# Optimization experiments

Measured on AMD Instinct MI355X. Metric: run time of the kernel, lower is better.

Reference implementation:

```python
import jax, jax.numpy as jnp
import numpy as np

NUM_HEADS = 16


def setup_inputs() -> dict:
    key = jax.random.key(0)
    ks = jax.random.split(key, 7)
    B, L, H = 4, 1370, 1024
    s = 0.02
    return {
        "hidden_states": jax.random.normal(ks[0], (B, L, H), jnp.float32),
        "Wq": jax.random.normal(ks[1], (H, H), jnp.float32) * s,
        "bq": jax.random.normal(ks[2], (H,), jnp.float32) * s,
        "Wk": jax.random.normal(ks[3], (H, H), jnp.float32) * s,
        "bk": jax.random.normal(ks[4], (H,), jnp.float32) * s,
        "Wv": jax.random.normal(ks[5], (H, H), jnp.float32) * s,
        "bv": jax.random.normal(ks[6], (H,), jnp.float32) * s,
    }


def reference(hidden_states, Wq, bq, Wk, bk, Wv, bv):
    B, L, hidden = hidden_states.shape
    n_heads = NUM_HEADS
    d = hidden // n_heads  # head_dim = 64

    def split_heads(x):  # [B,L,hidden] -> [B,H,L,d]
        return x.reshape(B, L, n_heads, d).transpose(0, 2, 1, 3)

    # torch Linear: y = x @ W^T + b
    q = split_heads(hidden_states @ Wq.T + bq)
    k = split_heads(hidden_states @ Wk.T + bk)
    v = split_heads(hidden_states @ Wv.T + bv)

    scale = 1.0 / jnp.sqrt(jnp.asarray(d, hidden_states.dtype))
    # attn_bias is all-zeros (no causal mask, no head_mask) -> omitted
    scores = jnp.einsum("bhld,bhsd->bhls", q, k) * scale  # [B,H,L,S]
    attn = jax.nn.softmax(scores, axis=-1)
    # dropout_p = 0.0 (eval mode), callback is None
    ctx = jnp.einsum("bhls,bhsd->bhld", attn, v)  # [B,H,L,d]
    ctx = ctx.transpose(0, 2, 1, 3).reshape(B, L, hidden)
    return ctx
```

## Files before the change

### kernel.cpp

```cpp
#include <hip/hip_runtime.h>

#define B_    4
#define L_    1370
#define NH_   16
#define D_    64
#define HID_  1024
#define M_    (B_ * L_)
#define LPAD  1408

#define XB_OFF  0u
#define WB_OFF  5611520u
#define QW_OFF  8757248u
#define KW_OFF  14524416u
#define VT_OFF  20291584u

typedef __attribute__((ext_vector_type(8))) short bf16x8;
typedef __attribute__((ext_vector_type(4))) short bf16x4;
typedef __attribute__((ext_vector_type(4))) float f32x4;
typedef __attribute__((ext_vector_type(2))) unsigned int u32x2;

#define LOG2E   1.44269504089f
#define QSCALE  0.18033688011f
#define SOFT_M2 14.4269504089f

__device__ __forceinline__ unsigned short f2bf(float f) {
  unsigned int u = __builtin_bit_cast(unsigned int, f);
  u += 0x7FFFu + ((u >> 16) & 1u);
  return (unsigned short)(u >> 16);
}

__device__ __forceinline__ float fexp2(float x) {
#if __has_builtin(__builtin_amdgcn_exp2f)
  return __builtin_amdgcn_exp2f(x);
#else
  return exp2f(x);
#endif
}

__device__ __forceinline__ unsigned int pkbf(float a, float b) {
#if __has_builtin(__builtin_amdgcn_cvt_pk_bf16_f32)
  auto r = __builtin_amdgcn_cvt_pk_bf16_f32(a, b);
  return __builtin_bit_cast(unsigned int, r);
#else
  return (unsigned int)f2bf(a) | ((unsigned int)f2bf(b) << 16);
#endif
}

#define GLOAD16(gp, lp)                                                    \
  __builtin_amdgcn_global_load_lds(                                        \
      (const __attribute__((address_space(1))) unsigned int*)(gp),         \
      (__attribute__((address_space(3))) unsigned int*)(lp), 16, 0, 0)

#define XN4 ((M_ * HID_) / 4)
#define WN4 ((HID_ * HID_) / 4)
#define TOT4 (XN4 + 3 * WN4)

__global__ void cvt_all(const float* __restrict__ hs,
                        const float* __restrict__ Wq,
                        const float* __restrict__ Wk,
                        const float* __restrict__ Wv,
                        unsigned short* __restrict__ ws) {
  int i4 = blockIdx.x * 256 + threadIdx.x;
  if (i4 >= TOT4) return;
  const float* src;
  unsigned short* dst;
  if (i4 < XN4) {
    src = hs + (size_t)i4 * 4;
    dst = ws + XB_OFF + (size_t)i4 * 4;
  } else {
    int j = i4 - XN4;
    int w = j >> 18;
    int jj = j & (WN4 - 1);
    src = (w == 0 ? Wq : w == 1 ? Wk : Wv) + (size_t)jj * 4;
    dst = ws + WB_OFF + (size_t)w * (HID_ * HID_) + (size_t)jj * 4;
  }
  float4 v = *(const float4*)src;
  bf16x4 o;
  o[0] = (short)f2bf(v.x); o[1] = (short)f2bf(v.y);
  o[2] = (short)f2bf(v.z); o[3] = (short)f2bf(v.w);
  *(bf16x4*)dst = o;
}

__global__ __launch_bounds__(256)
void qkv_gemm(const unsigned short* __restrict__ XB,
              const unsigned short* __restrict__ WB,
              const float* __restrict__ bq,
              const float* __restrict__ bk,
              const float* __restrict__ bv,
              unsigned short* __restrict__ ws) {
  __shared__ unsigned short smem[16384];
  unsigned short* lA = smem;
  unsigned short* lB = smem + 8192;

  const int x = blockIdx.x;
  const int b = (x >= 33) ? 3 : (x >= 22) ? 2 : (x >= 11) ? 1 : 0;
  const int j = x - 11 * b;
  const int z = blockIdx.z;
  const int n0 = blockIdx.y * 128;

  const unsigned short* W = WB + (size_t)z * (HID_ * HID_);
  const float* bias = (z == 0) ? bq : (z == 1) ? bk : bv;
  const float scale = (z == 0) ? QSCALE : 1.0f;

  const int tid = threadIdx.x;
  const int lane = tid & 63;
  const int wv = tid >> 6;
  const int l15 = lane & 15, quad = lane >> 4;
  const int wr = wv >> 1, wc = wv & 1;

  const int srow = (lane >> 3);
  const int gsw = (lane & 7) ^ srow;
  int offA[4], offB[4];
#pragma unroll
  for (int i = 0; i < 4; ++i) {
    int row = wv * 32 + 8 * i + srow;
    int m = b * L_ + min(j * 128 + row, L_ - 1);
    offA[i] = m * HID_ + gsw * 8;
    offB[i] = (n0 + row) * HID_ + gsw * 8;
  }

  f32x4 acc[4][4];
#pragma unroll
  for (int i = 0; i < 4; i++)
#pragma unroll
    for (int jj = 0; jj < 4; jj++) acc[i][jj] = (f32x4){0.f, 0.f, 0.f, 0.f};

  for (int kt = 0; kt < HID_ / 64; ++kt) {
    __syncthreads();
#pragma unroll
    for (int i = 0; i < 4; ++i) {
      GLOAD16(XB + offA[i] + kt * 64, &lA[(wv * 32 + 8 * i) * 64]);
      GLOAD16(W + offB[i] + kt * 64, &lB[(wv * 32 + 8 * i) * 64]);
    }
    __syncthreads();
#pragma unroll
    for (int kk = 0; kk < 2; ++kk) {
      bf16x8 af[4], bfr[4];
#pragma unroll
      for (int mi = 0; mi < 4; mi++) {
        int row = wr * 64 + mi * 16 + l15;
        af[mi] = *(const bf16x8*)&lA[row * 64 + (((kk * 4 + quad) ^ (l15 & 7)) * 8)];
      }
#pragma unroll
      for (int ni = 0; ni < 4; ni++) {
        int row = wc * 64 + ni * 16 + l15;
        bfr[ni] = *(const bf16x8*)&lB[row * 64 + (((kk * 4 + quad) ^ (l15 & 7)) * 8)];
      }
#pragma unroll
      for (int mi = 0; mi < 4; mi++)
#pragma unroll
        for (int ni = 0; ni < 4; ni++)
          acc[mi][ni] = __builtin_amdgcn_mfma_f32_16x16x32_bf16(af[mi], bfr[ni], acc[mi][ni], 0, 0, 0);
    }
  }

  __syncthreads();
  unsigned short* lC = smem + wv * 4096;
  const int h = blockIdx.y * 2 + wc;
  const int bh = b * 16 + h;
  const int lbase = j * 128 + wr * 64;

  if (z < 2) {
#pragma unroll
    for (int ni = 0; ni < 4; ni++) {
      int nl = ni * 16 + l15;
      float bn = bias[n0 + wc * 64 + nl];
      int gsn = nl >> 3, en = nl & 7;
#pragma unroll
      for (int mi = 0; mi < 4; mi++)
#pragma unroll
        for (int r = 0; r < 4; r++) {
          int ml = mi * 16 + quad * 4 + r;
          lC[ml * 64 + ((gsn ^ (ml & 7)) * 8) + en] = f2bf((acc[mi][ni][r] + bn) * scale);
        }
    }
    unsigned short* dst = ws + (z == 0 ? QW_OFF : KW_OFF) + (size_t)bh * (LPAD * 64);
#pragma unroll
    for (int i = 0; i < 8; ++i) {
      int ml = i * 8 + (lane >> 3);
      int g = lane & 7;
      bf16x8 v = *(const bf16x8*)&lC[ml * 64 + ((g ^ (ml & 7)) * 8)];
      int l = lbase + ml;
      *(bf16x8*)(dst + (size_t)l * 64 + g * 8) = v;
    }
  } else {
#pragma unroll
    for (int ni = 0; ni < 4; ni++) {
      int nl = ni * 16 + l15;
      float bn = bias[n0 + wc * 64 + nl];
#pragma unroll
      for (int mi = 0; mi < 4; mi++) {
        bf16x4 pk;
#pragma unroll
        for (int r = 0; r < 4; r++) pk[r] = (short)f2bf(acc[mi][ni][r] + bn);
        int gm = mi * 2 + (quad >> 1), h2 = quad & 1;
        *(bf16x4*)&lC[nl * 64 + ((gm ^ (nl & 7)) * 8) + h2 * 4] = pk;
      }
    }
    unsigned short* vt = ws + VT_OFF + (size_t)bh * (64 * LPAD);
#pragma unroll
    for (int i = 0; i < 8; ++i) {
      int nl = i * 8 + (lane >> 3);
      int g = lane & 7;
      bf16x8 v = *(const bf16x8*)&lC[nl * 64 + ((g ^ (nl & 7)) * 8)];
      int l = lbase + g * 8;
      *(bf16x8*)(vt + (size_t)nl * LPAD + l) = v;
    }
  }
}

__global__ __launch_bounds__(256)
void attn(const unsigned short* __restrict__ ws, float* __restrict__ out) {
  __shared__ unsigned short lK[64 * 64];
  __shared__ unsigned short lV[64 * 64];
  __shared__ unsigned short lP[4 * 32 * 64];

  const int tid = threadIdx.x;
  const int qt = blockIdx.x >> 3;
  const int bh = blockIdx.y * 8 + (blockIdx.x & 7);
  const int b = bh >> 4, h = bh & 15;
  const int lane = tid & 63, wv = tid >> 6;
  const int l15 = lane & 15, quad = lane >> 4;

  const unsigned short* Qp = ws + QW_OFF + (size_t)bh * (LPAD * 64);
  const unsigned short* Kp = ws + KW_OFF + (size_t)bh * (LPAD * 64);
  const unsigned short* Vt = ws + VT_OFF + (size_t)bh * (64 * LPAD);

  const int srow = lane >> 3;
  const int gsw = (lane & 7) ^ srow;
  const bool isK = (wv < 2);
  const int half = wv & 1;
  const unsigned short* gbase = isK ? Kp : Vt;
  unsigned short* ldst = isK ? lK : lV;
  int goff[4];
#pragma unroll
  for (int t = 0; t < 4; ++t) {
    int row = half * 32 + 8 * t + srow;
    goff[t] = isK ? (row * 64 + gsw * 8)
                  : (row * LPAD + gsw * 8);
  }
  const int gstep = isK ? (64 * 64) : 64;

  bf16x8 qf[2][2];
#pragma unroll
  for (int q2 = 0; q2 < 2; ++q2) {
    int qrow = qt * 128 + wv * 32 + q2 * 16 + l15;
    qf[q2][0] = *(const bf16x8*)(Qp + (size_t)qrow * 64 + quad * 8);
    qf[q2][1] = *(const bf16x8*)(Qp + (size_t)qrow * 64 + 32 + quad * 8);
  }

  bf16x8 ones;
#pragma unroll
  for (int jj = 0; jj < 8; jj++) ones[jj] = (short)0x3F80;

  const f32x4 minit = {-SOFT_M2, -SOFT_M2, -SOFT_M2, -SOFT_M2};

  f32x4 o[2][4], osum[2];
#pragma unroll
  for (int q2 = 0; q2 < 2; q2++) {
    osum[q2] = (f32x4){0.f, 0.f, 0.f, 0.f};
#pragma unroll
    for (int d = 0; d < 4; d++) o[q2][d] = (f32x4){0.f, 0.f, 0.f, 0.f};
  }

  unsigned short* lPw = lP + wv * 2048;

  const int NT = (L_ + 63) / 64;
  for (int kt = 0; kt < NT; ++kt) {
    const int s0 = kt * 64;
    __syncthreads();
#pragma unroll
    for (int t = 0; t < 4; ++t)
      GLOAD16(gbase + goff[t] + kt * gstep, ldst + (half * 32 + 8 * t) * 64);
    __syncthreads();

#pragma unroll
    for (int cb = 0; cb < 4; cb++) {
      int krow = cb * 16 + l15;
      bf16x8 kf0 = *(const bf16x8*)&lK[krow * 64 + ((quad ^ (l15 & 7)) * 8)];
      bf16x8 kf1 = *(const bf16x8*)&lK[krow * 64 + (((4 + quad) ^ (l15 & 7)) * 8)];
#pragma unroll
      for (int q2 = 0; q2 < 2; q2++) {
        f32x4 a = minit;
        a = __builtin_amdgcn_mfma_f32_16x16x32_bf16(kf0, qf[q2][0], a, 0, 0, 0);
        a = __builtin_amdgcn_mfma_f32_16x16x32_bf16(kf1, qf[q2][1], a, 0, 0, 0);
        if (s0 + 64 > L_) {
#pragma unroll
          for (int r = 0; r < 4; r++)
            if (s0 + cb * 16 + quad * 4 + r >= L_) a[r] = -1e30f;
        }
        u32x2 pk;
        pk[0] = pkbf(fexp2(a[0]), fexp2(a[1]));
        pk[1] = pkbf(fexp2(a[2]), fexp2(a[3]));
        int prow = q2 * 16 + l15;
        int gw = cb * 2 + (quad >> 1), h2 = quad & 1;
        *(u32x2*)&lPw[prow * 64 + ((gw ^ (l15 & 7)) * 8) + h2 * 4] = pk;
      }
    }

#pragma unroll
    for (int kk = 0; kk < 2; kk++) {
      bf16x8 pa[2];
#pragma unroll
      for (int q2 = 0; q2 < 2; q2++) {
        pa[q2] = *(const bf16x8*)&lPw[(q2 * 16 + l15) * 64 + (((kk * 4 + quad) ^ (l15 & 7)) * 8)];
        osum[q2] = __builtin_amdgcn_mfma_f32_16x16x32_bf16(pa[q2], ones, osum[q2], 0, 0, 0);
      }
#pragma unroll
      for (int d = 0; d < 4; d++) {
        int vrow = d * 16 + l15;
        bf16x8 vb = *(const bf16x8*)&lV[vrow * 64 + (((kk * 4 + quad) ^ (l15 & 7)) * 8)];
#pragma unroll
        for (int q2 = 0; q2 < 2; q2++)
          o[q2][d] = __builtin_amdgcn_mfma_f32_16x16x32_bf16(pa[q2], vb, o[q2][d], 0, 0, 0);
      }
    }
  }

#pragma unroll
  for (int q2 = 0; q2 < 2; q2++) {
    float inv[4];
#pragma unroll
    for (int r = 0; r < 4; r++) inv[r] = 1.0f / osum[q2][r];
#pragma unroll
    for (int d = 0; d < 4; d++)
#pragma unroll
      for (int r = 0; r < 4; r++) {
        int l = qt * 128 + wv * 32 + q2 * 16 + quad * 4 + r;
        if (l < L_) {
          int dd = d * 16 + l15;
          out[((size_t)(b * L_ + l)) * HID_ + h * 64 + dd] = o[q2][d][r] * inv[r];
        }
      }
  }
}

extern "C" void kernel_launch(void* const* d_in, const int* in_sizes, int n_in,
                              void* d_out, int out_size, void* d_ws, size_t ws_size,
                              hipStream_t stream) {
  const float* hs = (const float*)d_in[0];
  const float* Wq = (const float*)d_in[1];
  const float* bq = (const float*)d_in[2];
  const float* Wk = (const float*)d_in[3];
  const float* bk = (const float*)d_in[4];
  const float* Wv = (const float*)d_in[5];
  const float* bv = (const float*)d_in[6];
  float* out = (float*)d_out;
  unsigned short* ws = (unsigned short*)d_ws;

  cvt_all<<<dim3((TOT4 + 255) / 256), 256, 0, stream>>>(hs, Wq, Wk, Wv, ws);

  qkv_gemm<<<dim3(44, 8, 3), 256, 0, stream>>>(ws + XB_OFF, ws + WB_OFF,
                                               bq, bk, bv, ws);

  attn<<<dim3(88, 8), 256, 0, stream>>>(ws, out);
}
```

Baseline: 206.5 us.

## Double GEMM K-tile to 128 and give attention waves 64 query rows

The QKV GEMM now stages 128-wide K slices in LDS, using a 16-way XOR swizzle and 64 KB of shared memory. This halves the number of barrier-separated load phases. The attention kernel drops from 4 waves to 2 waves per block, and each wave handles 64 query rows, so every K/V fragment read from LDS feeds twice as many MFMAs. The cost is many more accumulator registers per wave and fewer waves per block to hide latency, which may lower occupancy.

```diff
diff --git a/kernel.cpp b/kernel.cpp
--- a/kernel.cpp
+++ b/kernel.cpp
@@ -88,9 +88,9 @@
               const float* __restrict__ bk,
               const float* __restrict__ bv,
               unsigned short* __restrict__ ws) {
-  __shared__ unsigned short smem[16384];
+  __shared__ unsigned short smem[32768];
   unsigned short* lA = smem;
-  unsigned short* lB = smem + 8192;
+  unsigned short* lB = smem + 16384;
 
   const int x = blockIdx.x;
   const int b = (x >= 33) ? 3 : (x >= 22) ? 2 : (x >= 11) ? 1 : 0;
@@ -108,15 +108,16 @@
   const int l15 = lane & 15, quad = lane >> 4;
   const int wr = wv >> 1, wc = wv & 1;
 
-  const int srow = (lane >> 3);
-  const int gsw = (lane & 7) ^ srow;
-  int offA[4], offB[4];
-#pragma unroll
-  for (int i = 0; i < 4; ++i) {
-    int row = wv * 32 + 8 * i + srow;
+  const int crow = lane >> 4;
+  const int cg = lane & 15;
+  int offA[8], offB[8];
+#pragma unroll
+  for (int i = 0; i < 8; ++i) {
+    int row = wv * 32 + i * 4 + crow;
+    int g = cg ^ (row & 15);
     int m = b * L_ + min(j * 128 + row, L_ - 1);
-    offA[i] = m * HID_ + gsw * 8;
-    offB[i] = (n0 + row) * HID_ + gsw * 8;
+    offA[i] = m * HID_ + g * 8;
+    offB[i] = (n0 + row) * HID_ + g * 8;
   }
 
   f32x4 acc[4][4];
@@ -125,26 +126,26 @@
 #pragma unroll
     for (int jj = 0; jj < 4; jj++) acc[i][jj] = (f32x4){0.f, 0.f, 0.f, 0.f};
 
-  for (int kt = 0; kt < HID_ / 64; ++kt) {
+  for (int kt = 0; kt < HID_ / 128; ++kt) {
     __syncthreads();
 #pragma unroll
-    for (int i = 0; i < 4; ++i) {
-      GLOAD16(XB + offA[i] + kt * 64, &lA[(wv * 32 + 8 * i) * 64]);
-      GLOAD16(W + offB[i] + kt * 64, &lB[(wv * 32 + 8 * i) * 64]);
+    for (int i = 0; i < 8; ++i) {
+      GLOAD16(XB + offA[i] + kt * 128, &lA[(wv * 32 + i * 4) * 128]);
+      GLOAD16(W + offB[i] + kt * 128, &lB[(wv * 32 + i * 4) * 128]);
     }
     __syncthreads();
 #pragma unroll
-    for (int kk = 0; kk < 2; ++kk) {
+    for (int kk = 0; kk < 4; ++kk) {
       bf16x8 af[4], bfr[4];
 #pragma unroll
       for (int mi = 0; mi < 4; mi++) {
         int row = wr * 64 + mi * 16 + l15;
-        af[mi] = *(const bf16x8*)&lA[row * 64 + (((kk * 4 + quad) ^ (l15 & 7)) * 8)];
+        af[mi] = *(const bf16x8*)&lA[row * 128 + (((kk * 4 + quad) ^ l15) * 8)];
       }
 #pragma unroll
       for (int ni = 0; ni < 4; ni++) {
         int row = wc * 64 + ni * 16 + l15;
-        bfr[ni] = *(const bf16x8*)&lB[row * 64 + (((kk * 4 + quad) ^ (l15 & 7)) * 8)];
+        bfr[ni] = *(const bf16x8*)&lB[row * 128 + (((kk * 4 + quad) ^ l15) * 8)];
       }
 #pragma unroll
       for (int mi = 0; mi < 4; mi++)
@@ -209,11 +210,11 @@
   }
 }
 
-__global__ __launch_bounds__(256)
+__global__ __launch_bounds__(128)
 void attn(const unsigned short* __restrict__ ws, float* __restrict__ out) {
   __shared__ unsigned short lK[64 * 64];
   __shared__ unsigned short lV[64 * 64];
-  __shared__ unsigned short lP[4 * 32 * 64];
+  __shared__ unsigned short lP[2 * 64 * 64];
 
   const int tid = threadIdx.x;
   const int qt = blockIdx.x >> 3;
@@ -228,23 +229,21 @@
 
   const int srow = lane >> 3;
   const int gsw = (lane & 7) ^ srow;
-  const bool isK = (wv < 2);
-  const int half = wv & 1;
-  const unsigned short* gbase = isK ? Kp : Vt;
-  unsigned short* ldst = isK ? lK : lV;
-  int goff[4];
-#pragma unroll
-  for (int t = 0; t < 4; ++t) {
-    int row = half * 32 + 8 * t + srow;
-    goff[t] = isK ? (row * 64 + gsw * 8)
-                  : (row * LPAD + gsw * 8);
-  }
-  const int gstep = isK ? (64 * 64) : 64;
-
-  bf16x8 qf[2][2];
-#pragma unroll
-  for (int q2 = 0; q2 < 2; ++q2) {
-    int qrow = qt * 128 + wv * 32 + q2 * 16 + l15;
+  const unsigned short* gbase = (wv == 0) ? Kp : Vt;
+  unsigned short* ldst = (wv == 0) ? lK : lV;
+  int goff[8];
+#pragma unroll
+  for (int t = 0; t < 8; ++t) {
+    int row = 8 * t + srow;
+    goff[t] = (wv == 0) ? (row * 64 + gsw * 8)
+                        : (row * LPAD + gsw * 8);
+  }
+  const int gstep = (wv == 0) ? (64 * 64) : 64;
+
+  bf16x8 qf[4][2];
+#pragma unroll
+  for (int q2 = 0; q2 < 4; ++q2) {
+    int qrow = qt * 128 + wv * 64 + q2 * 16 + l15;
     qf[q2][0] = *(const bf16x8*)(Qp + (size_t)qrow * 64 + quad * 8);
     qf[q2][1] = *(const bf16x8*)(Qp + (size_t)qrow * 64 + 32 + quad * 8);
   }
@@ -255,23 +254,23 @@
 
   const f32x4 minit = {-SOFT_M2, -SOFT_M2, -SOFT_M2, -SOFT_M2};
 
-  f32x4 o[2][4], osum[2];
-#pragma unroll
-  for (int q2 = 0; q2 < 2; q2++) {
+  f32x4 o[4][4], osum[4];
+#pragma unroll
+  for (int q2 = 0; q2 < 4; q2++) {
     osum[q2] = (f32x4){0.f, 0.f, 0.f, 0.f};
 #pragma unroll
     for (int d = 0; d < 4; d++) o[q2][d] = (f32x4){0.f, 0.f, 0.f, 0.f};
   }
 
-  unsigned short* lPw = lP + wv * 2048;
+  unsigned short* lPw = lP + wv * 4096;
 
   const int NT = (L_ + 63) / 64;
   for (int kt = 0; kt < NT; ++kt) {
     const int s0 = kt * 64;
     __syncthreads();
 #pragma unroll
-    for (int t = 0; t < 4; ++t)
-      GLOAD16(gbase + goff[t] + kt * gstep, ldst + (half * 32 + 8 * t) * 64);
+    for (int t = 0; t < 8; ++t)
+      GLOAD16(gbase + goff[t] + kt * gstep, ldst + t * 512);
     __syncthreads();
 
 #pragma unroll
@@ -280,7 +279,7 @@
       bf16x8 kf0 = *(const bf16x8*)&lK[krow * 64 + ((quad ^ (l15 & 7)) * 8)];
       bf16x8 kf1 = *(const bf16x8*)&lK[krow * 64 + (((4 + quad) ^ (l15 & 7)) * 8)];
 #pragma unroll
-      for (int q2 = 0; q2 < 2; q2++) {
+      for (int q2 = 0; q2 < 4; q2++) {
         f32x4 a = minit;
         a = __builtin_amdgcn_mfma_f32_16x16x32_bf16(kf0, qf[q2][0], a, 0, 0, 0);
         a = __builtin_amdgcn_mfma_f32_16x16x32_bf16(kf1, qf[q2][1], a, 0, 0, 0);
@@ -300,9 +299,9 @@
 
 #pragma unroll
     for (int kk = 0; kk < 2; kk++) {
-      bf16x8 pa[2];
-#pragma unroll
-      for (int q2 = 0; q2 < 2; q2++) {
+      bf16x8 pa[4];
+#pragma unroll
+      for (int q2 = 0; q2 < 4; q2++) {
         pa[q2] = *(const bf16x8*)&lPw[(q2 * 16 + l15) * 64 + (((kk * 4 + quad) ^ (l15 & 7)) * 8)];
         osum[q2] = __builtin_amdgcn_mfma_f32_16x16x32_bf16(pa[q2], ones, osum[q2], 0, 0, 0);
       }
@@ -311,14 +310,14 @@
         int vrow = d * 16 + l15;
         bf16x8 vb = *(const bf16x8*)&lV[vrow * 64 + (((kk * 4 + quad) ^ (l15 & 7)) * 8)];
 #pragma unroll
-        for (int q2 = 0; q2 < 2; q2++)
+        for (int q2 = 0; q2 < 4; q2++)
           o[q2][d] = __builtin_amdgcn_mfma_f32_16x16x32_bf16(pa[q2], vb, o[q2][d], 0, 0, 0);
       }
     }
   }
 
 #pragma unroll
-  for (int q2 = 0; q2 < 2; q2++) {
+  for (int q2 = 0; q2 < 4; q2++) {
     float inv[4];
 #pragma unroll
     for (int r = 0; r < 4; r++) inv[r] = 1.0f / osum[q2][r];
@@ -326,7 +325,7 @@
     for (int d = 0; d < 4; d++)
 #pragma unroll
       for (int r = 0; r < 4; r++) {
-        int l = qt * 128 + wv * 32 + q2 * 16 + quad * 4 + r;
+        int l = qt * 128 + wv * 64 + q2 * 16 + quad * 4 + r;
         if (l < L_) {
           int dd = d * 16 + l15;
           out[((size_t)(b * L_ + l)) * HID_ + h * 64 + dd] = o[q2][d][r] * inv[r];
@@ -353,5 +352,5 @@
   qkv_gemm<<<dim3(44, 8, 3), 256, 0, stream>>>(ws + XB_OFF, ws + WB_OFF,
                                                bq, bk, bv, ws);
 
-  attn<<<dim3(88, 8), 256, 0, stream>>>(ws, out);
-}
+  attn<<<dim3(88, 8), 128, 0, stream>>>(ws, out);
+}
```

Result: slower. 271.6 us (+31.5%).

## Double-buffer LDS tiles in QKV GEMM and attention kernels

Applied to the files above, without the earlier changes.

Both the QKV projection GEMM and the attention kernel now keep two LDS buffers. Each loop iteration issues the global-to-LDS copy for the next K tile (or K/V block) before computing on the current one, which removes one barrier per iteration. The aim is to hide global load latency behind MFMA work. In exchange, LDS use doubles per block (64 KB for the GEMM, 48 KB for attention), which may lower the number of blocks resident per CU.

```diff
diff --git a/kernel.cpp b/kernel.cpp
--- a/kernel.cpp
+++ b/kernel.cpp
@@ -88,9 +88,7 @@
               const float* __restrict__ bk,
               const float* __restrict__ bv,
               unsigned short* __restrict__ ws) {
-  __shared__ unsigned short smem[16384];
-  unsigned short* lA = smem;
-  unsigned short* lB = smem + 8192;
+  __shared__ unsigned short smem[32768];
 
   const int x = blockIdx.x;
   const int b = (x >= 33) ? 3 : (x >= 22) ? 2 : (x >= 11) ? 1 : 0;
@@ -125,14 +123,26 @@
 #pragma unroll
     for (int jj = 0; jj < 4; jj++) acc[i][jj] = (f32x4){0.f, 0.f, 0.f, 0.f};
 
+#pragma unroll
+  for (int i = 0; i < 4; ++i) {
+    GLOAD16(XB + offA[i], &smem[(wv * 32 + 8 * i) * 64]);
+    GLOAD16(W + offB[i], &smem[8192 + (wv * 32 + 8 * i) * 64]);
+  }
+
   for (int kt = 0; kt < HID_ / 64; ++kt) {
     __syncthreads();
-#pragma unroll
-    for (int i = 0; i < 4; ++i) {
-      GLOAD16(XB + offA[i] + kt * 64, &lA[(wv * 32 + 8 * i) * 64]);
-      GLOAD16(W + offB[i] + kt * 64, &lB[(wv * 32 + 8 * i) * 64]);
-    }
-    __syncthreads();
+    unsigned short* cur = smem + (kt & 1) * 16384;
+    if (kt + 1 < HID_ / 64) {
+      unsigned short* nxt = smem + ((kt + 1) & 1) * 16384;
+      const int ko = (kt + 1) * 64;
+#pragma unroll
+      for (int i = 0; i < 4; ++i) {
+        GLOAD16(XB + offA[i] + ko, &nxt[(wv * 32 + 8 * i) * 64]);
+        GLOAD16(W + offB[i] + ko, &nxt[8192 + (wv * 32 + 8 * i) * 64]);
+      }
+    }
+    const unsigned short* lA = cur;
+    const unsigned short* lB = cur + 8192;
 #pragma unroll
     for (int kk = 0; kk < 2; ++kk) {
       bf16x8 af[4], bfr[4];
@@ -211,8 +221,7 @@
 
 __global__ __launch_bounds__(256)
 void attn(const unsigned short* __restrict__ ws, float* __restrict__ out) {
-  __shared__ unsigned short lK[64 * 64];
-  __shared__ unsigned short lV[64 * 64];
+  __shared__ unsigned short lKV[2 * 8192];
   __shared__ unsigned short lP[4 * 32 * 64];
 
   const int tid = threadIdx.x;
@@ -231,7 +240,7 @@
   const bool isK = (wv < 2);
   const int half = wv & 1;
   const unsigned short* gbase = isK ? Kp : Vt;
-  unsigned short* ldst = isK ? lK : lV;
+  const int lofs = (isK ? 0 : 4096) + half * 32 * 64;
   int goff[4];
 #pragma unroll
   for (int t = 0; t < 4; ++t) {
@@ -266,13 +275,23 @@
   unsigned short* lPw = lP + wv * 2048;
 
   const int NT = (L_ + 63) / 64;
+
+#pragma unroll
+  for (int t = 0; t < 4; ++t)
+    GLOAD16(gbase + goff[t], lKV + lofs + t * 512);
+
   for (int kt = 0; kt < NT; ++kt) {
     const int s0 = kt * 64;
     __syncthreads();
-#pragma unroll
-    for (int t = 0; t < 4; ++t)
-      GLOAD16(gbase + goff[t] + kt * gstep, ldst + (half * 32 + 8 * t) * 64);
-    __syncthreads();
+    const unsigned short* lK = lKV + (kt & 1) * 8192;
+    const unsigned short* lV = lK + 4096;
+    if (kt + 1 < NT) {
+      unsigned short* nxt = lKV + ((kt + 1) & 1) * 8192 + lofs;
+      const int go = (kt + 1) * gstep;
+#pragma unroll
+      for (int t = 0; t < 4; ++t)
+        GLOAD16(gbase + goff[t] + go, nxt + t * 512);
+    }
 
 #pragma unroll
     for (int cb = 0; cb < 4; cb++) {
```

After: 194.0 us. 1.06x faster.
